# Kernel tuning notes

Measured on AMD Instinct MI355X. Metric: run time of the kernel, lower is better.

## Reference

```python
import jax, jax.numpy as jnp
import numpy as np

DIM = 128
IND_DIM = 5
HEADS = 4
DIM_HEAD = 32
HIDDEN = HEADS * DIM_HEAD  # 128
SCALE = DIM_HEAD ** -0.5


def setup_inputs() -> dict:
    key = jax.random.key(0)
    ks = jax.random.split(key, 6)
    b, n = 1, 512
    x = jax.random.normal(ks[0], (b, DIM, n), dtype=jnp.float32)
    indicator = jax.random.normal(ks[1], (b, IND_DIM, n, n), dtype=jnp.float32)
    # conv1d kernels with kernel_size=1 are just (out, in) matrices
    w_qkv = jax.random.normal(ks[2], (HIDDEN * 3, DIM), dtype=jnp.float32) * (DIM ** -0.5)
    w_ind = jax.random.normal(ks[3], (HIDDEN * 2, IND_DIM), dtype=jnp.float32) * (IND_DIM ** -0.5)
    w_out = jax.random.normal(ks[4], (DIM, HIDDEN), dtype=jnp.float32) * (HIDDEN ** -0.5)
    b_out = jax.random.normal(ks[5], (DIM,), dtype=jnp.float32) * 0.01
    return {"x": x, "indicator": indicator, "w_qkv": w_qkv,
            "w_ind": w_ind, "w_out": w_out, "b_out": b_out}


def reference(x, indicator, w_qkv, w_ind, w_out, b_out):
    b, c, n = x.shape
    h, dh = HEADS, DIM_HEAD
    # pointwise conv = channel matmul
    qkv = jnp.einsum('oc,bcn->bon', w_qkv, x)  # (b, 3*hidden, n)
    q, k, v = jnp.split(qkv, 3, axis=1)
    q = q.reshape(b, h, dh, n)
    k = k.reshape(b, h, dh, n)
    v = v.reshape(b, h, dh, n)
    ind = jnp.einsum('oc,bcij->boij', w_ind, indicator)  # (b, 2*hidden, n, n)
    ind_q, ind_k = jnp.split(ind, 2, axis=1)
    ind_q = ind_q.reshape(b, h, dh, n, n)
    ind_k = ind_k.reshape(b, h, dh, n, n)
    qq = (q[..., :, None] + ind_q) * SCALE        # (b, h, dh, n, n)
    kk = k[..., None, :] + ind_k                   # (b, h, dh, n, n)
    sim = jnp.einsum('bhdij,bhdij->bhij', qq, kk)  # (b, h, n, n)
    attn = jax.nn.softmax(sim, axis=-1)
    out = jnp.einsum('bhij,bhdj->bhdi', attn, v)   # (b, h, dh, n)
    out = out.reshape(b, h * dh, n)
    return jnp.einsum('oc,bcn->bon', w_out, out) + b_out[None, :, None]
```

## Files before the change

### kernel.cpp

```cpp
#include <hip/hip_runtime.h>
#include <hip/hip_fp16.h>
#include <math.h>

#define N      512
#define DIMC   128
#define HEADS  4
#define DH     32
#define INDC   5
#define SCALE  0.1767766952966369f

#define QKV_ROWS 384
#define AQ_BASE  384
#define AK_BASE  404
#define TOT_ROWS 424
#define NROW_BLK (TOT_ROWS / 4)

#define MHS_F    (TOT_ROWS * N / 2)
#define WOUTT_F  (MHS_F + 64)

__global__ __launch_bounds__(256) void pre_kernel(const float* __restrict__ w_qkv,
                                                  const float* __restrict__ w_ind,
                                                  const float* __restrict__ x,
                                                  const float* __restrict__ w_out,
                                                  float* __restrict__ ws) {
    const int bx = blockIdx.x;
    const int t  = threadIdx.x;
    __half* rows  = (__half*)ws;
    float* MhS    = ws + MHS_F;
    float* w_outT = ws + WOUTT_F;

    if (bx == NROW_BLK) {
        if (blockIdx.y != 0) return;
        __shared__ float mraw[HEADS * INDC * INDC];
        if (t < HEADS * INDC * INDC) {
            const int h = t / 25, c = (t / 5) % 5, cc = t % 5;
            float acc = 0.f;
            for (int d = 0; d < DH; ++d)
                acc = fmaf(w_ind[(h * DH + d) * INDC + c],
                           w_ind[(DIMC + h * DH + d) * INDC + cc], acc);
            mraw[t] = acc;
        }
        __syncthreads();
        if (t < 64) {
            const int h = t >> 4, idx = t & 15;
            const int PC[10]  = {0, 0, 0, 0, 1, 1, 1, 2, 2, 3};
            const int PCC[10] = {1, 2, 3, 4, 2, 3, 4, 3, 4, 4};
            float s = 0.f;
            if (idx < 5) {
                s = mraw[h * 25 + idx * 5 + idx];
            } else if (idx < 15) {
                const int c = PC[idx - 5], cc = PCC[idx - 5];
                s = mraw[h * 25 + c * 5 + cc] + mraw[h * 25 + cc * 5 + c];
            }
            MhS[h * 16 + idx] = s;
        }
        for (int idx = t; idx < DIMC * DIMC; idx += 256) {
            const int o = idx >> 7, c = idx & 127;
            w_outT[c * DIMC + o] = w_out[idx];
        }
        return;
    }

    __shared__ float ws2[4 * DIMC];
    const int o0 = bx * 4;
    for (int idx = t; idx < 4 * DIMC; idx += 256) {
        const int r = idx & 3, m = idx >> 2;
        const int row = o0 + r;
        float val;
        if (row < QKV_ROWS) {
            val = w_qkv[row * DIMC + m];
        } else if (row < AK_BASE) {
            const int rr = row - AQ_BASE, h = rr / INDC, c = rr % INDC;
            float acc = 0.f;
            for (int d = 0; d < DH; ++d)
                acc = fmaf(w_qkv[(h * DH + d) * DIMC + m],
                           w_ind[(DIMC + h * DH + d) * INDC + c], acc);
            val = acc;
        } else {
            const int rr = row - AK_BASE, h = rr / INDC, c = rr % INDC;
            float acc = 0.f;
            for (int d = 0; d < DH; ++d)
                acc = fmaf(w_qkv[(DIMC + h * DH + d) * DIMC + m],
                           w_ind[(h * DH + d) * INDC + c], acc);
            val = acc;
        }
        ws2[m * 4 + r] = val;
    }
    __syncthreads();

    const int i = blockIdx.y * 256 + t;
    float acc[4] = {0.f, 0.f, 0.f, 0.f};
#pragma unroll 8
    for (int c = 0; c < DIMC; ++c) {
        const float xv = x[c * N + i];
        const float4 wv = *(const float4*)(ws2 + c * 4);
        acc[0] = fmaf(wv.x, xv, acc[0]);
        acc[1] = fmaf(wv.y, xv, acc[1]);
        acc[2] = fmaf(wv.z, xv, acc[2]);
        acc[3] = fmaf(wv.w, xv, acc[3]);
    }
#pragma unroll
    for (int r = 0; r < 4; ++r) rows[(o0 + r) * N + i] = __float2half(acc[r]);
}

__global__ __launch_bounds__(256) void attn_kernel(const float* __restrict__ ws,
                                                   const float* __restrict__ ind,
                                                   const float* __restrict__ b_out,
                                                   float* __restrict__ out) {
    const int i0   = blockIdx.x * 2;
    const int t    = threadIdx.x;
    const int lane = t & 63;
    const int h    = t >> 6;

    const __half* rows  = (const __half*)ws;
    const float* MhS    = ws + MHS_F;
    const float* w_outT = ws + WOUTT_F;

    __shared__ float qs[2][DIMC];
    __shared__ float aqs[2][HEADS * INDC];
    __shared__ float msS[HEADS * 16];
    __shared__ float red[HEADS][DH][64];
    __shared__ float attv[2][DIMC];
    __shared__ float outred[4][2][DIMC];

    float4 ic0[2][INDC], ic1[2][INDC];
#pragma unroll
    for (int s = 0; s < 2; ++s) {
        const int g = lane + 64 * s;
#pragma unroll
        for (int c = 0; c < INDC; ++c) {
            ic0[s][c] = ((const float4*)(ind + (c * N + i0) * N))[g];
            ic1[s][c] = ((const float4*)(ind + (c * N + i0 + 1) * N))[g];
        }
    }

    const __half* q  = rows;
    const __half* Aq = rows + 3 * DIMC * N;
    if (t < DIMC) qs[0][t] = __half2float(q[t * N + i0]);
    else          qs[1][t - DIMC] = __half2float(q[(t - DIMC) * N + i0 + 1]);
    if (t < 2 * HEADS * INDC) {
        const int ii = t / (HEADS * INDC), r = t % (HEADS * INDC);
        aqs[ii][r] = __half2float(Aq[r * N + i0 + ii]);
    } else if (t < 2 * HEADS * INDC + 64) {
        msS[t - 2 * HEADS * INDC] = MhS[t - 2 * HEADS * INDC];
    }
    __syncthreads();

    const float2* k4  = (const float2*)(rows + DIMC * N);
    const float2* v4  = (const float2*)(rows + 2 * DIMC * N);
    const float2* Ak4 = (const float2*)(rows + (3 * DIMC + HEADS * INDC) * N);

    float4 sr0[2], sr1[2];
    float m0 = -1e30f, m1 = -1e30f;
#pragma unroll
    for (int s = 0; s < 2; ++s) {
        const int g = lane + 64 * s;
        float4 a0 = {0.f, 0.f, 0.f, 0.f}, a1 = {0.f, 0.f, 0.f, 0.f};
#pragma unroll
        for (int d = 0; d < DH; ++d) {
            const float2 raw = k4[(h * DH + d) * 128 + g];
            const float2 fa = __half22float2(*(const __half2*)&raw.x);
            const float2 fb = __half22float2(*(const __half2*)&raw.y);
            const float q0 = qs[0][h * DH + d], q1 = qs[1][h * DH + d];
            a0.x = fmaf(q0, fa.x, a0.x); a0.y = fmaf(q0, fa.y, a0.y);
            a0.z = fmaf(q0, fb.x, a0.z); a0.w = fmaf(q0, fb.y, a0.w);
            a1.x = fmaf(q1, fa.x, a1.x); a1.y = fmaf(q1, fa.y, a1.y);
            a1.z = fmaf(q1, fb.x, a1.z); a1.w = fmaf(q1, fb.y, a1.w);
        }
#pragma unroll
        for (int c = 0; c < INDC; ++c) {
            const float2 raw = Ak4[(h * INDC + c) * 128 + g];
            const float2 fa = __half22float2(*(const __half2*)&raw.x);
            const float2 fb = __half22float2(*(const __half2*)&raw.y);
            const float b0 = aqs[0][h * INDC + c], b1 = aqs[1][h * INDC + c];
            const float4 v0 = ic0[s][c], v1 = ic1[s][c];
            a0.x = fmaf(b0 + fa.x, v0.x, a0.x); a0.y = fmaf(b0 + fa.y, v0.y, a0.y);
            a0.z = fmaf(b0 + fb.x, v0.z, a0.z); a0.w = fmaf(b0 + fb.y, v0.w, a0.w);
            a1.x = fmaf(b1 + fa.x, v1.x, a1.x); a1.y = fmaf(b1 + fa.y, v1.y, a1.y);
            a1.z = fmaf(b1 + fb.x, v1.z, a1.z); a1.w = fmaf(b1 + fb.y, v1.w, a1.w);
        }
        const int PCf[15]  = {0, 1, 2, 3, 4, 0, 0, 0, 0, 1, 1, 1, 2, 2, 3};
        const int PCCf[15] = {0, 1, 2, 3, 4, 1, 2, 3, 4, 2, 3, 4, 3, 4, 4};
#pragma unroll
        for (int p = 0; p < 15; ++p) {
            const float sv = msS[h * 16 + p];
            const float4 A0 = ic0[s][PCf[p]], B0 = ic0[s][PCCf[p]];
            const float4 A1 = ic1[s][PCf[p]], B1 = ic1[s][PCCf[p]];
            a0.x = fmaf(sv, A0.x * B0.x, a0.x); a0.y = fmaf(sv, A0.y * B0.y, a0.y);
            a0.z = fmaf(sv, A0.z * B0.z, a0.z); a0.w = fmaf(sv, A0.w * B0.w, a0.w);
            a1.x = fmaf(sv, A1.x * B1.x, a1.x); a1.y = fmaf(sv, A1.y * B1.y, a1.y);
            a1.z = fmaf(sv, A1.z * B1.z, a1.z); a1.w = fmaf(sv, A1.w * B1.w, a1.w);
        }
        sr0[s] = make_float4(SCALE * a0.x, SCALE * a0.y, SCALE * a0.z, SCALE * a0.w);
        sr1[s] = make_float4(SCALE * a1.x, SCALE * a1.y, SCALE * a1.z, SCALE * a1.w);
        m0 = fmaxf(m0, fmaxf(fmaxf(sr0[s].x, sr0[s].y), fmaxf(sr0[s].z, sr0[s].w)));
        m1 = fmaxf(m1, fmaxf(fmaxf(sr1[s].x, sr1[s].y), fmaxf(sr1[s].z, sr1[s].w)));
    }

#pragma unroll
    for (int off = 1; off < 64; off <<= 1) {
        m0 = fmaxf(m0, __shfl_xor(m0, off, 64));
        m1 = fmaxf(m1, __shfl_xor(m1, off, 64));
    }
    float4 e0[2], e1[2];
    float sum0 = 0.f, sum1 = 0.f;
#pragma unroll
    for (int s = 0; s < 2; ++s) {
        e0[s].x = __expf(sr0[s].x - m0); e0[s].y = __expf(sr0[s].y - m0);
        e0[s].z = __expf(sr0[s].z - m0); e0[s].w = __expf(sr0[s].w - m0);
        e1[s].x = __expf(sr1[s].x - m1); e1[s].y = __expf(sr1[s].y - m1);
        e1[s].z = __expf(sr1[s].z - m1); e1[s].w = __expf(sr1[s].w - m1);
        sum0 += (e0[s].x + e0[s].y) + (e0[s].z + e0[s].w);
        sum1 += (e1[s].x + e1[s].y) + (e1[s].z + e1[s].w);
    }
#pragma unroll
    for (int off = 1; off < 64; off <<= 1) {
        sum0 += __shfl_xor(sum0, off, 64);
        sum1 += __shfl_xor(sum1, off, 64);
    }
    const float r0 = 1.f / sum0, r1 = 1.f / sum1;

    float acc0[DH], acc1[DH];
#pragma unroll
    for (int d = 0; d < DH; ++d) { acc0[d] = 0.f; acc1[d] = 0.f; }
#pragma unroll
    for (int s = 0; s < 2; ++s) {
        const int g = lane + 64 * s;
        const float4 p0 = e0[s], p1 = e1[s];
#pragma unroll
        for (int d = 0; d < DH; ++d) {
            const float2 raw = v4[(h * DH + d) * 128 + g];
            const float2 fa = __half22float2(*(const __half2*)&raw.x);
            const float2 fb = __half22float2(*(const __half2*)&raw.y);
            acc0[d] = fmaf(p0.x, fa.x, fmaf(p0.y, fa.y,
                      fmaf(p0.z, fb.x, fmaf(p0.w, fb.y, acc0[d]))));
            acc1[d] = fmaf(p1.x, fa.x, fmaf(p1.y, fa.y,
                      fmaf(p1.z, fb.x, fmaf(p1.w, fb.y, acc1[d]))));
        }
    }

    {
        const int d = lane & 31, half = lane >> 5;
#pragma unroll
        for (int dd = 0; dd < DH; ++dd) red[h][dd][lane ^ dd] = acc0[dd];
        float s = 0.f;
#pragma unroll
        for (int kk = 0; kk < 32; ++kk) s += red[h][d][(half * 32 + kk) ^ d];
        s += __shfl_down(s, 32, 64);
        if (lane < 32) attv[0][h * DH + d] = s * r0;
#pragma unroll
        for (int dd = 0; dd < DH; ++dd) red[h][dd][lane ^ dd] = acc1[dd];
        s = 0.f;
#pragma unroll
        for (int kk = 0; kk < 32; ++kk) s += red[h][d][(half * 32 + kk) ^ d];
        s += __shfl_down(s, 32, 64);
        if (lane < 32) attv[1][h * DH + d] = s * r1;
    }
    __syncthreads();

    {
        const int po = t & 63;
        const int quarter = t >> 6;
        const float2* wT2 = (const float2*)w_outT;
        float2 a0 = {0.f, 0.f}, a1 = {0.f, 0.f};
#pragma unroll 8
        for (int c = quarter * 32; c < quarter * 32 + 32; ++c) {
            const float2 wv = wT2[c * 64 + po];
            const float av0 = attv[0][c], av1 = attv[1][c];
            a0.x = fmaf(wv.x, av0, a0.x); a0.y = fmaf(wv.y, av0, a0.y);
            a1.x = fmaf(wv.x, av1, a1.x); a1.y = fmaf(wv.y, av1, a1.y);
        }
        ((float2*)&outred[quarter][0][0])[po] = a0;
        ((float2*)&outred[quarter][1][0])[po] = a1;
    }
    __syncthreads();
    {
        const int o = t & 127, ii = t >> 7;
        out[o * N + i0 + ii] = ((outred[0][ii][o] + outred[1][ii][o]) +
                                (outred[2][ii][o] + outred[3][ii][o])) + b_out[o];
    }
}

extern "C" void kernel_launch(void* const* d_in, const int* in_sizes, int n_in,
                              void* d_out, int out_size, void* d_ws, size_t ws_size,
                              hipStream_t stream) {
    const float* x         = (const float*)d_in[0];
    const float* indicator = (const float*)d_in[1];
    const float* w_qkv     = (const float*)d_in[2];
    const float* w_ind     = (const float*)d_in[3];
    const float* w_out     = (const float*)d_in[4];
    const float* b_out     = (const float*)d_in[5];
    float* out = (float*)d_out;
    float* ws  = (float*)d_ws;

    pre_kernel<<<dim3(NROW_BLK + 1, 2), 256, 0, stream>>>(w_qkv, w_ind, x, w_out, ws);
    attn_kernel<<<N / 2, 256, 0, stream>>>(ws, indicator, b_out, out);
}
```

Baseline: 98.38 us.

## Split attention block into one wave per (query row, head) with 512 threads

The attention kernel goes from 256 to 512 threads per block, so each wave handles a single query row and head instead of two query rows. This halves per-thread registers (one score set, one accumulator array) and doubles waves available to hide the latency of the half-precision K/V loads. The cross-lane reduction of the value accumulator now uses a shuffle before a smaller shared-memory transpose, and the output projection is split across 8 wave groups. The cost is that each K, V and Ak element is now loaded twice per block (once per query row wave) instead of once, doubling L2/global traffic for those rows.

```diff
diff --git a/kernel.cpp b/kernel.cpp
--- a/kernel.cpp
+++ b/kernel.cpp
@@ -103,14 +103,17 @@
     for (int r = 0; r < 4; ++r) rows[(o0 + r) * N + i] = __float2half(acc[r]);
 }
 
-__global__ __launch_bounds__(256) void attn_kernel(const float* __restrict__ ws,
+__global__ __launch_bounds__(512) void attn_kernel(const float* __restrict__ ws,
                                                    const float* __restrict__ ind,
                                                    const float* __restrict__ b_out,
                                                    float* __restrict__ out) {
     const int i0   = blockIdx.x * 2;
     const int t    = threadIdx.x;
     const int lane = t & 63;
-    const int h    = t >> 6;
+    const int w    = t >> 6;
+    const int h    = w & 3;
+    const int ii   = w >> 2;
+    const int i    = i0 + ii;
 
     const __half* rows  = (const __half*)ws;
     const float* MhS    = ws + MHS_F;
@@ -119,30 +122,32 @@
     __shared__ float qs[2][DIMC];
     __shared__ float aqs[2][HEADS * INDC];
     __shared__ float msS[HEADS * 16];
-    __shared__ float red[HEADS][DH][64];
+    __shared__ float red[8][DH][32];
     __shared__ float attv[2][DIMC];
-    __shared__ float outred[4][2][DIMC];
-
-    float4 ic0[2][INDC], ic1[2][INDC];
+    __shared__ float outred[8][2][DIMC];
+
+    float4 ic[2][INDC];
 #pragma unroll
     for (int s = 0; s < 2; ++s) {
         const int g = lane + 64 * s;
 #pragma unroll
-        for (int c = 0; c < INDC; ++c) {
-            ic0[s][c] = ((const float4*)(ind + (c * N + i0) * N))[g];
-            ic1[s][c] = ((const float4*)(ind + (c * N + i0 + 1) * N))[g];
-        }
+        for (int c = 0; c < INDC; ++c)
+            ic[s][c] = ((const float4*)(ind + (c * N + i) * N))[g];
     }
 
     const __half* q  = rows;
     const __half* Aq = rows + 3 * DIMC * N;
-    if (t < DIMC) qs[0][t] = __half2float(q[t * N + i0]);
-    else          qs[1][t - DIMC] = __half2float(q[(t - DIMC) * N + i0 + 1]);
-    if (t < 2 * HEADS * INDC) {
-        const int ii = t / (HEADS * INDC), r = t % (HEADS * INDC);
-        aqs[ii][r] = __half2float(Aq[r * N + i0 + ii]);
-    } else if (t < 2 * HEADS * INDC + 64) {
-        msS[t - 2 * HEADS * INDC] = MhS[t - 2 * HEADS * INDC];
+    if (t < DIMC) {
+        qs[0][t] = __half2float(q[t * N + i0]);
+    } else if (t < 2 * DIMC) {
+        qs[1][t - DIMC] = __half2float(q[(t - DIMC) * N + i0 + 1]);
+    } else if (t < 2 * DIMC + 2 * HEADS * INDC) {
+        const int r2 = t - 2 * DIMC;
+        const int iw = r2 / (HEADS * INDC), r = r2 % (HEADS * INDC);
+        aqs[iw][r] = __half2float(Aq[r * N + i0 + iw]);
+    } else if (t < 2 * DIMC + 2 * HEADS * INDC + 64) {
+        const int r = t - 2 * DIMC - 2 * HEADS * INDC;
+        msS[r] = MhS[r];
     }
     __syncthreads();
 
@@ -150,134 +155,117 @@
     const float2* v4  = (const float2*)(rows + 2 * DIMC * N);
     const float2* Ak4 = (const float2*)(rows + (3 * DIMC + HEADS * INDC) * N);
 
-    float4 sr0[2], sr1[2];
-    float m0 = -1e30f, m1 = -1e30f;
+    float4 sr[2];
+    float m = -1e30f;
 #pragma unroll
     for (int s = 0; s < 2; ++s) {
         const int g = lane + 64 * s;
-        float4 a0 = {0.f, 0.f, 0.f, 0.f}, a1 = {0.f, 0.f, 0.f, 0.f};
+        float4 a = {0.f, 0.f, 0.f, 0.f};
 #pragma unroll
         for (int d = 0; d < DH; ++d) {
             const float2 raw = k4[(h * DH + d) * 128 + g];
             const float2 fa = __half22float2(*(const __half2*)&raw.x);
             const float2 fb = __half22float2(*(const __half2*)&raw.y);
-            const float q0 = qs[0][h * DH + d], q1 = qs[1][h * DH + d];
-            a0.x = fmaf(q0, fa.x, a0.x); a0.y = fmaf(q0, fa.y, a0.y);
-            a0.z = fmaf(q0, fb.x, a0.z); a0.w = fmaf(q0, fb.y, a0.w);
-            a1.x = fmaf(q1, fa.x, a1.x); a1.y = fmaf(q1, fa.y, a1.y);
-            a1.z = fmaf(q1, fb.x, a1.z); a1.w = fmaf(q1, fb.y, a1.w);
+            const float qv = qs[ii][h * DH + d];
+            a.x = fmaf(qv, fa.x, a.x); a.y = fmaf(qv, fa.y, a.y);
+            a.z = fmaf(qv, fb.x, a.z); a.w = fmaf(qv, fb.y, a.w);
         }
 #pragma unroll
         for (int c = 0; c < INDC; ++c) {
             const float2 raw = Ak4[(h * INDC + c) * 128 + g];
             const float2 fa = __half22float2(*(const __half2*)&raw.x);
             const float2 fb = __half22float2(*(const __half2*)&raw.y);
-            const float b0 = aqs[0][h * INDC + c], b1 = aqs[1][h * INDC + c];
-            const float4 v0 = ic0[s][c], v1 = ic1[s][c];
-            a0.x = fmaf(b0 + fa.x, v0.x, a0.x); a0.y = fmaf(b0 + fa.y, v0.y, a0.y);
-            a0.z = fmaf(b0 + fb.x, v0.z, a0.z); a0.w = fmaf(b0 + fb.y, v0.w, a0.w);
-            a1.x = fmaf(b1 + fa.x, v1.x, a1.x); a1.y = fmaf(b1 + fa.y, v1.y, a1.y);
-            a1.z = fmaf(b1 + fb.x, v1.z, a1.z); a1.w = fmaf(b1 + fb.y, v1.w, a1.w);
+            const float b0 = aqs[ii][h * INDC + c];
+            const float4 v0 = ic[s][c];
+            a.x = fmaf(b0 + fa.x, v0.x, a.x); a.y = fmaf(b0 + fa.y, v0.y, a.y);
+            a.z = fmaf(b0 + fb.x, v0.z, a.z); a.w = fmaf(b0 + fb.y, v0.w, a.w);
         }
         const int PCf[15]  = {0, 1, 2, 3, 4, 0, 0, 0, 0, 1, 1, 1, 2, 2, 3};
         const int PCCf[15] = {0, 1, 2, 3, 4, 1, 2, 3, 4, 2, 3, 4, 3, 4, 4};
 #pragma unroll
         for (int p = 0; p < 15; ++p) {
             const float sv = msS[h * 16 + p];
-            const float4 A0 = ic0[s][PCf[p]], B0 = ic0[s][PCCf[p]];
-            const float4 A1 = ic1[s][PCf[p]], B1 = ic1[s][PCCf[p]];
-            a0.x = fmaf(sv, A0.x * B0.x, a0.x); a0.y = fmaf(sv, A0.y * B0.y, a0.y);
-            a0.z = fmaf(sv, A0.z * B0.z, a0.z); a0.w = fmaf(sv, A0.w * B0.w, a0.w);
-            a1.x = fmaf(sv, A1.x * B1.x, a1.x); a1.y = fmaf(sv, A1.y * B1.y, a1.y);
-            a1.z = fmaf(sv, A1.z * B1.z, a1.z); a1.w = fmaf(sv, A1.w * B1.w, a1.w);
-        }
-        sr0[s] = make_float4(SCALE * a0.x, SCALE * a0.y, SCALE * a0.z, SCALE * a0.w);
-        sr1[s] = make_float4(SCALE * a1.x, SCALE * a1.y, SCALE * a1.z, SCALE * a1.w);
-        m0 = fmaxf(m0, fmaxf(fmaxf(sr0[s].x, sr0[s].y), fmaxf(sr0[s].z, sr0[s].w)));
-        m1 = fmaxf(m1, fmaxf(fmaxf(sr1[s].x, sr1[s].y), fmaxf(sr1[s].z, sr1[s].w)));
-    }
-
-#pragma unroll
-    for (int off = 1; off < 64; off <<= 1) {
-        m0 = fmaxf(m0, __shfl_xor(m0, off, 64));
-        m1 = fmaxf(m1, __shfl_xor(m1, off, 64));
-    }
-    float4 e0[2], e1[2];
-    float sum0 = 0.f, sum1 = 0.f;
-#pragma unroll
-    for (int s = 0; s < 2; ++s) {
-        e0[s].x = __expf(sr0[s].x - m0); e0[s].y = __expf(sr0[s].y - m0);
-        e0[s].z = __expf(sr0[s].z - m0); e0[s].w = __expf(sr0[s].w - m0);
-        e1[s].x = __expf(sr1[s].x - m1); e1[s].y = __expf(sr1[s].y - m1);
-        e1[s].z = __expf(sr1[s].z - m1); e1[s].w = __expf(sr1[s].w - m1);
-        sum0 += (e0[s].x + e0[s].y) + (e0[s].z + e0[s].w);
-        sum1 += (e1[s].x + e1[s].y) + (e1[s].z + e1[s].w);
-    }
-#pragma unroll
-    for (int off = 1; off < 64; off <<= 1) {
-        sum0 += __shfl_xor(sum0, off, 64);
-        sum1 += __shfl_xor(sum1, off, 64);
-    }
-    const float r0 = 1.f / sum0, r1 = 1.f / sum1;
-
-    float acc0[DH], acc1[DH];
-#pragma unroll
-    for (int d = 0; d < DH; ++d) { acc0[d] = 0.f; acc1[d] = 0.f; }
+            const float4 A = ic[s][PCf[p]], B = ic[s][PCCf[p]];
+            a.x = fmaf(sv, A.x * B.x, a.x); a.y = fmaf(sv, A.y * B.y, a.y);
+            a.z = fmaf(sv, A.z * B.z, a.z); a.w = fmaf(sv, A.w * B.w, a.w);
+        }
+        sr[s] = make_float4(SCALE * a.x, SCALE * a.y, SCALE * a.z, SCALE * a.w);
+        m = fmaxf(m, fmaxf(fmaxf(sr[s].x, sr[s].y), fmaxf(sr[s].z, sr[s].w)));
+    }
+
+#pragma unroll
+    for (int off = 1; off < 64; off <<= 1)
+        m = fmaxf(m, __shfl_xor(m, off, 64));
+    float4 e[2];
+    float sum = 0.f;
+#pragma unroll
+    for (int s = 0; s < 2; ++s) {
+        e[s].x = __expf(sr[s].x - m); e[s].y = __expf(sr[s].y - m);
+        e[s].z = __expf(sr[s].z - m); e[s].w = __expf(sr[s].w - m);
+        sum += (e[s].x + e[s].y) + (e[s].z + e[s].w);
+    }
+#pragma unroll
+    for (int off = 1; off < 64; off <<= 1)
+        sum += __shfl_xor(sum, off, 64);
+    const float rnorm = 1.f / sum;
+
+    float acc[DH];
+#pragma unroll
+    for (int d = 0; d < DH; ++d) acc[d] = 0.f;
 #pragma unroll
     for (int s = 0; s < 2; ++s) {
         const int g = lane + 64 * s;
-        const float4 p0 = e0[s], p1 = e1[s];
+        const float4 p = e[s];
 #pragma unroll
         for (int d = 0; d < DH; ++d) {
             const float2 raw = v4[(h * DH + d) * 128 + g];
             const float2 fa = __half22float2(*(const __half2*)&raw.x);
             const float2 fb = __half22float2(*(const __half2*)&raw.y);
-            acc0[d] = fmaf(p0.x, fa.x, fmaf(p0.y, fa.y,
-                      fmaf(p0.z, fb.x, fmaf(p0.w, fb.y, acc0[d]))));
-            acc1[d] = fmaf(p1.x, fa.x, fmaf(p1.y, fa.y,
-                      fmaf(p1.z, fb.x, fmaf(p1.w, fb.y, acc1[d]))));
+            acc[d] = fmaf(p.x, fa.x, fmaf(p.y, fa.y,
+                     fmaf(p.z, fb.x, fmaf(p.w, fb.y, acc[d]))));
         }
     }
 
     {
-        const int d = lane & 31, half = lane >> 5;
-#pragma unroll
-        for (int dd = 0; dd < DH; ++dd) red[h][dd][lane ^ dd] = acc0[dd];
-        float s = 0.f;
-#pragma unroll
-        for (int kk = 0; kk < 32; ++kk) s += red[h][d][(half * 32 + kk) ^ d];
-        s += __shfl_down(s, 32, 64);
-        if (lane < 32) attv[0][h * DH + d] = s * r0;
-#pragma unroll
-        for (int dd = 0; dd < DH; ++dd) red[h][dd][lane ^ dd] = acc1[dd];
-        s = 0.f;
-#pragma unroll
-        for (int kk = 0; kk < 32; ++kk) s += red[h][d][(half * 32 + kk) ^ d];
-        s += __shfl_down(s, 32, 64);
-        if (lane < 32) attv[1][h * DH + d] = s * r1;
+#pragma unroll
+        for (int d = 0; d < DH; ++d)
+            acc[d] += __shfl_xor(acc[d], 32, 64);
+        const int l5 = lane & 31;
+        if (lane < 32) {
+#pragma unroll
+            for (int dd = 0; dd < DH; ++dd) red[w][dd][l5 ^ dd] = acc[dd];
+        }
+        if (lane < 32) {
+            float s = 0.f;
+#pragma unroll
+            for (int kk = 0; kk < 32; ++kk) s += red[w][l5][kk ^ l5];
+            attv[ii][h * DH + l5] = s * rnorm;
+        }
     }
     __syncthreads();
 
     {
-        const int po = t & 63;
-        const int quarter = t >> 6;
+        const int po  = t & 63;
+        const int grp = t >> 6;
         const float2* wT2 = (const float2*)w_outT;
         float2 a0 = {0.f, 0.f}, a1 = {0.f, 0.f};
-#pragma unroll 8
-        for (int c = quarter * 32; c < quarter * 32 + 32; ++c) {
+#pragma unroll
+        for (int c = grp * 16; c < grp * 16 + 16; ++c) {
             const float2 wv = wT2[c * 64 + po];
             const float av0 = attv[0][c], av1 = attv[1][c];
             a0.x = fmaf(wv.x, av0, a0.x); a0.y = fmaf(wv.y, av0, a0.y);
             a1.x = fmaf(wv.x, av1, a1.x); a1.y = fmaf(wv.y, av1, a1.y);
         }
-        ((float2*)&outred[quarter][0][0])[po] = a0;
-        ((float2*)&outred[quarter][1][0])[po] = a1;
-    }
-    __syncthreads();
-    {
-        const int o = t & 127, ii = t >> 7;
-        out[o * N + i0 + ii] = ((outred[0][ii][o] + outred[1][ii][o]) +
-                                (outred[2][ii][o] + outred[3][ii][o])) + b_out[o];
+        ((float2*)&outred[grp][0][0])[po] = a0;
+        ((float2*)&outred[grp][1][0])[po] = a1;
+    }
+    __syncthreads();
+    if (t < 256) {
+        const int o = t & 127, iw = t >> 7;
+        float s = 0.f;
+#pragma unroll
+        for (int g = 0; g < 8; ++g) s += outred[g][iw][o];
+        out[o * N + i0 + iw] = s + b_out[o];
     }
 }
 
@@ -294,5 +282,5 @@
     float* ws  = (float*)d_ws;
 
     pre_kernel<<<dim3(NROW_BLK + 1, 2), 256, 0, stream>>>(w_qkv, w_ind, x, w_out, ws);
-    attn_kernel<<<N / 2, 256, 0, stream>>>(ws, indicator, b_out, out);
+    attn_kernel<<<N / 2, 512, 0, stream>>>(ws, indicator, b_out, out);
 }
```

After: 98.88 us. No clear change (+0.5%).
